# Kernel optimization log

Measured on AMD Instinct MI355X. Metric: run time of the kernel, lower is better.

Reference implementation:

```python
import jax, jax.numpy as jnp
import numpy as np

D_MODEL = 768
H = 12
D_K = D_MODEL // H
NEG = -1e9


def setup_inputs() -> dict:
    key = jax.random.key(0)
    ks = jax.random.split(key, 12)
    B, S = 1, 4096
    q = jax.random.normal(ks[0], (B, S, D_MODEL), dtype=jnp.float32)
    k = jax.random.normal(ks[1], (B, S, D_MODEL), dtype=jnp.float32)
    v = jax.random.normal(ks[2], (B, S, D_MODEL), dtype=jnp.float32)
    # causal mask, 1 = attend, 0 = masked (masked_fill on mask == 0)
    mask = jnp.tril(jnp.ones((S, S), dtype=jnp.int32))[None, None, :, :]
    scale = 1.0 / np.sqrt(D_MODEL)
    Wq = jax.random.normal(ks[3], (D_MODEL, D_MODEL), dtype=jnp.float32) * scale
    bq = jnp.zeros((D_MODEL,), dtype=jnp.float32)
    Wk = jax.random.normal(ks[4], (D_MODEL, D_MODEL), dtype=jnp.float32) * scale
    bk = jnp.zeros((D_MODEL,), dtype=jnp.float32)
    Wv = jax.random.normal(ks[5], (D_MODEL, D_MODEL), dtype=jnp.float32) * scale
    bv = jnp.zeros((D_MODEL,), dtype=jnp.float32)
    Wo = jax.random.normal(ks[6], (D_MODEL, D_MODEL), dtype=jnp.float32) * scale
    bo = jnp.zeros((D_MODEL,), dtype=jnp.float32)
    return {"q": q, "k": k, "v": v, "mask": mask,
            "Wq": Wq, "bq": bq, "Wk": Wk, "bk": bk,
            "Wv": Wv, "bv": bv, "Wo": Wo, "bo": bo}


def _split_heads(x):
    B, S, _ = x.shape
    return x.reshape(B, S, H, D_K).transpose(0, 2, 1, 3)  # [B,H,S,Dk]


def reference(q, k, v, mask, Wq, bq, Wk, bk, Wv, bv, Wo, bo):
    # Linear projections (torch Linear: x @ W.T + b; here W stored as [in,out])
    query = _split_heads(q @ Wq + bq)
    key = _split_heads(k @ Wk + bk)
    value = _split_heads(v @ Wv + bv)
    # scaled dot-product attention, full score matrix [B,H,Sq,Sk]
    scores = jnp.einsum("bhqd,bhkd->bhqk", query, key) / jnp.sqrt(
        jnp.asarray(D_K, dtype=query.dtype))
    scores = jnp.where(mask == 0, jnp.asarray(NEG, dtype=scores.dtype), scores)
    attn = jax.nn.softmax(scores, axis=-1)  # dropout p=0.0 -> identity
    x = jnp.einsum("bhqk,bhkd->bhqd", attn, value)
    B, _, S, _ = x.shape
    x = x.transpose(0, 2, 1, 3).reshape(B, S, H * D_K)
    return x @ Wo + bo
```

## Files before the change

kernel.cpp:

```cpp
#include <hip/hip_runtime.h>

typedef __bf16 bf16;
typedef __bf16 bf16x4 __attribute__((ext_vector_type(4)));
typedef __bf16 bf16x8 __attribute__((ext_vector_type(8)));
typedef float  floatx4 __attribute__((ext_vector_type(4)));

#define MFMA16(a,b,c) __builtin_amdgcn_mfma_f32_16x16x32_bf16((a),(b),(c),0,0,0)

static constexpr int S_LEN = 4096;
static constexpr int DM = 768;
static constexpr int NH = 12;
static constexpr int W_ELEMS = 768 * 768;
static constexpr int PARTS_PER_HEAD = 144;
static constexpr float CE = 0.18033688011112042f;

__device__ __forceinline__ void gld16(const bf16* g, bf16* l) {
    __builtin_amdgcn_global_load_lds(
        (const __attribute__((address_space(1))) void*)g,
        (__attribute__((address_space(3))) void*)l, 16, 0, 0);
}

__global__ __launch_bounds__(256) void prep_kernel(
    const float* __restrict__ q, const float* __restrict__ k, const float* __restrict__ v,
    const float* __restrict__ W0, const float* __restrict__ W1,
    const float* __restrict__ W2, const float* __restrict__ W3,
    bf16* Qc, bf16* Kc, bf16* Vc,
    bf16* T0, bf16* T1, bf16* T2, bf16* T3, int n)
{
    const int y = blockIdx.y;
    const int tid = threadIdx.x;
    if (y < 3) {
        const float* src = y == 0 ? q : (y == 1 ? k : v);
        bf16* dst = y == 0 ? Qc : (y == 1 ? Kc : Vc);
        int i = (blockIdx.x * 256 + tid) * 4;
        if (i < n) {
            float4 w = *(const float4*)&src[i];
            bf16x4 o; o[0] = (bf16)w.x; o[1] = (bf16)w.y; o[2] = (bf16)w.z; o[3] = (bf16)w.w;
            *(bf16x4*)&dst[i] = o;
        }
        return;
    }
    int x = blockIdx.x;
    if (x >= 576) return;
    const int mat = x / 144, t = x % 144;
    const float* W = mat == 0 ? W0 : (mat == 1 ? W1 : (mat == 2 ? W2 : W3));
    bf16* T = mat == 0 ? T0 : (mat == 1 ? T1 : (mat == 2 ? T2 : T3));
    const int k0 = (t / 12) * 64, n0 = (t % 12) * 64;
    __shared__ float Tl[64][65];
#pragma unroll
    for (int i = 0; i < 4; ++i) {
        int idx = i * 256 + tid;
        int r = idx >> 4, c4 = idx & 15;
        float4 w = *(const float4*)&W[(k0 + r) * 768 + n0 + c4 * 4];
        Tl[c4 * 4 + 0][r] = w.x; Tl[c4 * 4 + 1][r] = w.y;
        Tl[c4 * 4 + 2][r] = w.z; Tl[c4 * 4 + 3][r] = w.w;
    }
    __syncthreads();
#pragma unroll
    for (int i = 0; i < 4; ++i) {
        int idx = i * 256 + tid;
        int c = idx >> 4, r4 = idx & 15;
        bf16x4 o;
        o[0] = (bf16)Tl[c][r4 * 4 + 0]; o[1] = (bf16)Tl[c][r4 * 4 + 1];
        o[2] = (bf16)Tl[c][r4 * 4 + 2]; o[3] = (bf16)Tl[c][r4 * 4 + 3];
        *(bf16x4*)&T[(n0 + c) * 768 + k0 + r4 * 4] = o;
    }
}

template <bool OUT_F32>
__global__ __launch_bounds__(256) void gemm128_kernel(
    const bf16* __restrict__ A0, const bf16* __restrict__ A1, const bf16* __restrict__ A2,
    const bf16* __restrict__ B0, const bf16* __restrict__ B1, const bf16* __restrict__ B2,
    const float* __restrict__ c0, const float* __restrict__ c1, const float* __restrict__ c2,
    void* O0, void* O1, void* O2, int M, int N, int K, float qscale)
{
    const int z = blockIdx.z;
    const bf16* A = z == 0 ? A0 : (z == 1 ? A1 : A2);
    const bf16* B = z == 0 ? B0 : (z == 1 ? B1 : B2);
    const float* bias = z == 0 ? c0 : (z == 1 ? c1 : c2);
    void* C = z == 0 ? O0 : (z == 1 ? O1 : O2);
    const float osc = (z == 0) ? qscale : 1.0f;

    __shared__ bf16 As[2][128 * 64];
    __shared__ bf16 Bs[2][128 * 64];
    const int tid = threadIdx.x, lane = tid & 63, wave = tid >> 6;
    const int quad = lane >> 4, l16 = lane & 15, l8 = l16 & 7;
    const int rw = wave >> 1, cw = wave & 1;
    const int m0 = blockIdx.x * 128, n0 = blockIdx.y * 128;

    floatx4 acc[4][4] = {};

    auto stage = [&](int kt, int buf) {
#pragma unroll
        for (int i = 0; i < 4; ++i) {
            int ch = i * 256 + tid;
            int m = ch >> 3, kg = ch & 7;
            int kgd = kg ^ (m & 7);
            gld16(A + (size_t)(m0 + m) * K + kt * 64 + kgd * 8, &As[buf][ch * 8]);
        }
#pragma unroll
        for (int i = 0; i < 4; ++i) {
            int ch = i * 256 + tid;
            int n = ch >> 3, kg = ch & 7;
            int kgd = kg ^ (n & 7);
            gld16(B + (size_t)(n0 + n) * K + kt * 64 + kgd * 8, &Bs[buf][ch * 8]);
        }
    };

    const int NT = K >> 6;
    stage(0, 0);
    __syncthreads();

    for (int kt = 0; kt < NT; ++kt) {
        const int cur = kt & 1;
        if (kt + 1 < NT) stage(kt + 1, cur ^ 1);
#pragma unroll
        for (int ks = 0; ks < 2; ++ks) {
            bf16x8 a[4], b[4];
#pragma unroll
            for (int mt = 0; mt < 4; ++mt)
                a[mt] = *(const bf16x8*)&As[cur][(rw * 64 + mt * 16 + l16) * 64 + (((ks * 4 + quad) ^ l8) << 3)];
#pragma unroll
            for (int nt = 0; nt < 4; ++nt)
                b[nt] = *(const bf16x8*)&Bs[cur][(cw * 64 + nt * 16 + l16) * 64 + (((ks * 4 + quad) ^ l8) << 3)];
#pragma unroll
            for (int mt = 0; mt < 4; ++mt)
#pragma unroll
                for (int nt = 0; nt < 4; ++nt)
                    acc[mt][nt] = MFMA16(a[mt], b[nt], acc[mt][nt]);
        }
        __syncthreads();
    }
#pragma unroll
    for (int mt = 0; mt < 4; ++mt) {
        int row = m0 + rw * 64 + mt * 16 + quad * 4;
#pragma unroll
        for (int nt = 0; nt < 4; ++nt) {
            int col = n0 + cw * 64 + nt * 16 + l16;
            float bv = bias[col];
#pragma unroll
            for (int r = 0; r < 4; ++r) {
                float v = (acc[mt][nt][r] + bv) * osc;
                if (OUT_F32) ((float*)C)[(size_t)(row + r) * N + col] = v;
                else         ((bf16*)C)[(size_t)(row + r) * N + col] = (bf16)v;
            }
        }
    }
}

__global__ __launch_bounds__(256) void attn_kernel(
    const bf16* __restrict__ Q, const bf16* __restrict__ K,
    const bf16* __restrict__ V, float* __restrict__ Opart,
    float* __restrict__ Lpart)
{
    __shared__ bf16 Ps[128 * 64];
    __shared__ bf16 Ks[2][64 * 64];
    __shared__ bf16 Vt[64 * 64];

    const int h = blockIdx.y;
    const int idx = PARTS_PER_HEAD - 1 - (int)blockIdx.x;
    int g = 0;
    while (2 * (g + 1) * (g + 2) <= idx) ++g;
    const int rem = idx - 2 * g * (g + 1);
    const int qb = 4 * g + rem / (g + 1);
    const int c  = rem % (g + 1);
    const int ntiles = 2 * qb + 2;
    const int jstart = c * 8;
    const int jend   = (jstart + 8 < ntiles) ? jstart + 8 : ntiles;

    const int tid = threadIdx.x, lane = tid & 63, wave = tid >> 6;
    const int quad = lane >> 4, l16 = lane & 15, l8 = l16 & 7;
    const int qrow0 = qb * 128;
    const int cb = h * 64;

    auto stageK = [&](int j, int buf) {
#pragma unroll
        for (int i = 0; i < 2; ++i) {
            int ch = i * 256 + tid;
            int row = ch >> 3, kg = ch & 7;
            int kgd = kg ^ (row & 7);
            gld16(K + (size_t)(j * 64 + row) * DM + cb + kgd * 8, &Ks[buf][ch * 8]);
        }
    };
    auto loadV = [&](int j, bf16 vr[2][8]) {
#pragma unroll
        for (int i = 0; i < 2; ++i) {
            int kg = wave + i * 4;
#pragma unroll
            for (int u = 0; u < 8; ++u)
                vr[i][u] = V[(size_t)(j * 64 + kg * 8 + u) * DM + cb + lane];
        }
    };
    auto writeV = [&](bf16 vr[2][8]) {
#pragma unroll
        for (int i = 0; i < 2; ++i) {
            int kg = wave + i * 4;
            bf16x8 t;
#pragma unroll
            for (int u = 0; u < 8; ++u) t[u] = vr[i][u];
            *(bf16x8*)&Vt[lane * 64 + ((kg ^ (lane & 7)) << 3)] = t;
        }
    };

    bf16x8 qreg[2][2];
#pragma unroll
    for (int mt = 0; mt < 2; ++mt)
#pragma unroll
        for (int ks = 0; ks < 2; ++ks)
            qreg[mt][ks] = *(const bf16x8*)&Q[(size_t)(qrow0 + wave * 32 + mt * 16 + l16) * DM
                                             + cb + ks * 32 + quad * 8];

    stageK(jstart, 0);
    bf16 v0[2][8];
    loadV(jstart, v0);
    writeV(v0);
    __syncthreads();

    floatx4 o[2][4] = {};
    float lsum[2] = {0.f, 0.f};
    const int prowbase = (wave * 32 + l16) * 64;
    const int psub = (quad & 1) * 4;
    const int c16base = (quad >> 1);

    for (int j = jstart; j < jend; ++j) {
        const int cur = (j - jstart) & 1;
        bf16 vr[2][8];
        if (j + 1 < jend) {
            stageK(j + 1, cur ^ 1);
            loadV(j + 1, vr);
        }

        floatx4 st[2][4] = {};
#pragma unroll
        for (int ks = 0; ks < 2; ++ks) {
            bf16x8 kfr[4];
#pragma unroll
            for (int ct = 0; ct < 4; ++ct)
                kfr[ct] = *(const bf16x8*)&Ks[cur][(ct * 16 + l16) * 64 + (((ks * 4 + quad) ^ l8) << 3)];
#pragma unroll
            for (int mt = 0; mt < 2; ++mt)
#pragma unroll
                for (int ct = 0; ct < 4; ++ct)
                    st[mt][ct] = MFMA16(kfr[ct], qreg[mt][ks], st[mt][ct]);
        }

#pragma unroll
        for (int mt = 0; mt < 2; ++mt) {
            const int qs0 = qrow0 + wave * 32 + mt * 16;
            const int pb = prowbase + mt * 16 * 64;
            float lp = 0.f;
            if ((j * 64 + 63) <= qs0) {
#pragma unroll
                for (int ct = 0; ct < 4; ++ct) {
                    bf16x4 pk;
#pragma unroll
                    for (int r = 0; r < 4; ++r) {
                        float p = __builtin_amdgcn_exp2f(st[mt][ct][r]);
                        lp += p; pk[r] = (bf16)p;
                    }
                    *(bf16x4*)&Ps[pb + ((((ct * 2 + c16base) ^ l8) << 3) + psub)] = pk;
                }
            } else {
                const int qg = qs0 + l16;
#pragma unroll
                for (int ct = 0; ct < 4; ++ct) {
                    const int kg0 = j * 64 + ct * 16 + quad * 4;
                    bf16x4 pk;
#pragma unroll
                    for (int r = 0; r < 4; ++r) {
                        float p = (kg0 + r > qg) ? 0.f
                                  : __builtin_amdgcn_exp2f(st[mt][ct][r]);
                        lp += p; pk[r] = (bf16)p;
                    }
                    *(bf16x4*)&Ps[pb + ((((ct * 2 + c16base) ^ l8) << 3) + psub)] = pk;
                }
            }
            lsum[mt] += lp;
        }

#pragma unroll
        for (int ks = 0; ks < 2; ++ks) {
            bf16x8 bfr[4], afr[2];
#pragma unroll
            for (int ct = 0; ct < 4; ++ct)
                bfr[ct] = *(const bf16x8*)&Vt[(ct * 16 + l16) * 64 + (((ks * 4 + quad) ^ l8) << 3)];
#pragma unroll
            for (int mt = 0; mt < 2; ++mt)
                afr[mt] = *(const bf16x8*)&Ps[(wave * 32 + mt * 16 + l16) * 64 + (((ks * 4 + quad) ^ l8) << 3)];
#pragma unroll
            for (int mt = 0; mt < 2; ++mt)
#pragma unroll
                for (int ct = 0; ct < 4; ++ct)
                    o[mt][ct] = MFMA16(afr[mt], bfr[ct], o[mt][ct]);
        }

        if (j + 1 < jend) {
            __syncthreads();
            writeV(vr);
            __syncthreads();
        }
    }

    float* Op = Opart + (size_t)(h * PARTS_PER_HEAD + idx) * 128 * 64;
    float* Lp = Lpart + (size_t)(h * PARTS_PER_HEAD + idx) * 128;
#pragma unroll
    for (int mt = 0; mt < 2; ++mt) {
        float l = lsum[mt];
        l += __shfl_xor(l, 16);
        l += __shfl_xor(l, 32);
        if (lane < 16) Lp[wave * 32 + mt * 16 + l16] = l;
#pragma unroll
        for (int r = 0; r < 4; ++r) {
            const int rl = wave * 32 + mt * 16 + quad * 4 + r;
#pragma unroll
            for (int ct = 0; ct < 4; ++ct)
                Op[rl * 64 + ct * 16 + l16] = o[mt][ct][r];
        }
    }
}

__global__ __launch_bounds__(256) void attn_combine_kernel(
    const float* __restrict__ Opart, const float* __restrict__ Lpart,
    bf16* __restrict__ X)
{
    const int qb = blockIdx.x, h = blockIdx.y;
    const int g = qb >> 2;
    const int nc = g + 1;
    const int base = 2 * g * (g + 1) + (qb & 3) * (g + 1);
    const float* Op0 = Opart + (size_t)(h * PARTS_PER_HEAD + base) * 128 * 64;
    const float* Lp0 = Lpart + (size_t)(h * PARTS_PER_HEAD + base) * 128;

    for (int e = threadIdx.x * 4; e < 128 * 64; e += 1024) {
        const int row = e >> 6, col = e & 63;
        float4 acc = {0.f, 0.f, 0.f, 0.f};
        float l = 0.f;
        for (int p = 0; p < nc; ++p) {
            float4 w = *(const float4*)&Op0[p * 128 * 64 + e];
            acc.x += w.x; acc.y += w.y; acc.z += w.z; acc.w += w.w;
            l += Lp0[p * 128 + row];
        }
        const float rl = 1.0f / l;
        bf16x4 ov;
        ov[0] = (bf16)(acc.x * rl); ov[1] = (bf16)(acc.y * rl);
        ov[2] = (bf16)(acc.z * rl); ov[3] = (bf16)(acc.w * rl);
        *(bf16x4*)&X[(size_t)(qb * 128 + row) * DM + h * 64 + col] = ov;
    }
}

extern "C" void kernel_launch(void* const* d_in, const int* in_sizes, int n_in,
                              void* d_out, int out_size, void* d_ws, size_t ws_size,
                              hipStream_t stream)
{
    const float* q  = (const float*)d_in[0];
    const float* k  = (const float*)d_in[1];
    const float* v  = (const float*)d_in[2];
    const float* Wq = (const float*)d_in[4];
    const float* bq = (const float*)d_in[5];
    const float* Wk = (const float*)d_in[6];
    const float* bk = (const float*)d_in[7];
    const float* Wv = (const float*)d_in[8];
    const float* bv = (const float*)d_in[9];
    const float* Wo = (const float*)d_in[10];
    const float* bo = (const float*)d_in[11];

    const size_t NE = (size_t)S_LEN * DM;
    bf16* base = (bf16*)d_ws;
    bf16* Qp = base;
    bf16* Kp = base + NE;
    bf16* Vp = base + 2 * NE;
    bf16* Wt = base + 3 * NE;
    bf16 *Wqt = Wt, *Wkt = Wt + W_ELEMS, *Wvt = Wt + 2 * W_ELEMS, *Wot = Wt + 3 * W_ELEMS;
    bf16* scratch = Wt + 4 * W_ELEMS;
    bf16* Qc = scratch;
    bf16* Kc = scratch + NE;
    bf16* Vc = scratch + 2 * NE;
    float* Opart = (float*)scratch;
    float* Lpart = Opart + (size_t)NH * PARTS_PER_HEAD * 128 * 64;
    bf16* Xb = Qp;

    prep_kernel<<<dim3(3072, 4), 256, 0, stream>>>(
        q, k, v, Wq, Wk, Wv, Wo, Qc, Kc, Vc, Wqt, Wkt, Wvt, Wot, (int)NE);
    gemm128_kernel<false><<<dim3(32, 6, 3), 256, 0, stream>>>(
        Qc, Kc, Vc, Wqt, Wkt, Wvt, bq, bk, bv, Qp, Kp, Vp, S_LEN, DM, DM, CE);
    attn_kernel<<<dim3(PARTS_PER_HEAD, NH), 256, 0, stream>>>(Qp, Kp, Vp, Opart, Lpart);
    attn_combine_kernel<<<dim3(32, NH), 256, 0, stream>>>(Opart, Lpart, Xb);
    gemm128_kernel<true><<<dim3(32, 6, 1), 256, 0, stream>>>(
        Xb, Xb, Xb, Wot, Wot, Wot, bo, bo, bo, d_out, d_out, d_out, S_LEN, DM, DM, 1.0f);
}
```

Baseline: 276.5 us.

## Pre-transpose V globally and double-buffer V tiles via async LDS loads

Adds a separate kernel that transposes the projected V into a head-major [D, S] layout. The attention kernel can then stage V tiles with async global-to-LDS loads into a double buffer, just as it does for K. This removes the per-element scalar V loads, the register-to-LDS transpose writes and one of two barriers per iteration. Partial outputs are also stored in bf16 instead of fp32, which halves combine traffic at some precision cost, and the transpose adds an extra launch and a full pass over V.

```diff
diff --git a/kernel.cpp b/kernel.cpp
--- a/kernel.cpp
+++ b/kernel.cpp
@@ -67,6 +67,32 @@
     }
 }
 
+__global__ __launch_bounds__(256) void vtrans_kernel(
+    const bf16* __restrict__ Vp, bf16* __restrict__ VpT)
+{
+    __shared__ bf16 Tl[64][66];
+    const int tid = threadIdx.x;
+    const int r0 = blockIdx.x * 64, c0 = blockIdx.y * 64;
+#pragma unroll
+    for (int i = 0; i < 4; ++i) {
+        int idx = i * 256 + tid;
+        int r = idx >> 4, c4 = idx & 15;
+        bf16x4 w = *(const bf16x4*)&Vp[(size_t)(r0 + r) * DM + c0 + c4 * 4];
+        Tl[c4 * 4 + 0][r] = w[0]; Tl[c4 * 4 + 1][r] = w[1];
+        Tl[c4 * 4 + 2][r] = w[2]; Tl[c4 * 4 + 3][r] = w[3];
+    }
+    __syncthreads();
+#pragma unroll
+    for (int i = 0; i < 4; ++i) {
+        int idx = i * 256 + tid;
+        int c = idx >> 4, r4 = idx & 15;
+        bf16x4 o;
+        o[0] = Tl[c][r4 * 4 + 0]; o[1] = Tl[c][r4 * 4 + 1];
+        o[2] = Tl[c][r4 * 4 + 2]; o[3] = Tl[c][r4 * 4 + 3];
+        *(bf16x4*)&VpT[(size_t)(c0 + c) * S_LEN + r0 + r4 * 4] = o;
+    }
+}
+
 template <bool OUT_F32>
 __global__ __launch_bounds__(256) void gemm128_kernel(
     const bf16* __restrict__ A0, const bf16* __restrict__ A1, const bf16* __restrict__ A2,
@@ -150,12 +176,12 @@
 
 __global__ __launch_bounds__(256) void attn_kernel(
     const bf16* __restrict__ Q, const bf16* __restrict__ K,
-    const bf16* __restrict__ V, float* __restrict__ Opart,
+    const bf16* __restrict__ VpT, bf16* __restrict__ Opart,
     float* __restrict__ Lpart)
 {
     __shared__ bf16 Ps[128 * 64];
     __shared__ bf16 Ks[2][64 * 64];
-    __shared__ bf16 Vt[64 * 64];
+    __shared__ bf16 Vt[2][64 * 64];
 
     const int h = blockIdx.y;
     const int idx = PARTS_PER_HEAD - 1 - (int)blockIdx.x;
@@ -173,7 +199,7 @@
     const int qrow0 = qb * 128;
     const int cb = h * 64;
 
-    auto stageK = [&](int j, int buf) {
+    auto stageKV = [&](int j, int buf) {
 #pragma unroll
         for (int i = 0; i < 2; ++i) {
             int ch = i * 256 + tid;
@@ -181,24 +207,12 @@
             int kgd = kg ^ (row & 7);
             gld16(K + (size_t)(j * 64 + row) * DM + cb + kgd * 8, &Ks[buf][ch * 8]);
         }
-    };
-    auto loadV = [&](int j, bf16 vr[2][8]) {
 #pragma unroll
         for (int i = 0; i < 2; ++i) {
-            int kg = wave + i * 4;
-#pragma unroll
-            for (int u = 0; u < 8; ++u)
-                vr[i][u] = V[(size_t)(j * 64 + kg * 8 + u) * DM + cb + lane];
-        }
-    };
-    auto writeV = [&](bf16 vr[2][8]) {
-#pragma unroll
-        for (int i = 0; i < 2; ++i) {
-            int kg = wave + i * 4;
-            bf16x8 t;
-#pragma unroll
-            for (int u = 0; u < 8; ++u) t[u] = vr[i][u];
-            *(bf16x8*)&Vt[lane * 64 + ((kg ^ (lane & 7)) << 3)] = t;
+            int ch = i * 256 + tid;
+            int row = ch >> 3, kg = ch & 7;
+            int kgd = kg ^ (row & 7);
+            gld16(VpT + (size_t)(cb + row) * S_LEN + j * 64 + kgd * 8, &Vt[buf][ch * 8]);
         }
     };
 
@@ -210,10 +224,7 @@
             qreg[mt][ks] = *(const bf16x8*)&Q[(size_t)(qrow0 + wave * 32 + mt * 16 + l16) * DM
                                              + cb + ks * 32 + quad * 8];
 
-    stageK(jstart, 0);
-    bf16 v0[2][8];
-    loadV(jstart, v0);
-    writeV(v0);
+    stageKV(jstart, 0);
     __syncthreads();
 
     floatx4 o[2][4] = {};
@@ -224,11 +235,7 @@
 
     for (int j = jstart; j < jend; ++j) {
         const int cur = (j - jstart) & 1;
-        bf16 vr[2][8];
-        if (j + 1 < jend) {
-            stageK(j + 1, cur ^ 1);
-            loadV(j + 1, vr);
-        }
+        if (j + 1 < jend) stageKV(j + 1, cur ^ 1);
 
         floatx4 st[2][4] = {};
 #pragma unroll
@@ -283,7 +290,7 @@
             bf16x8 bfr[4], afr[2];
 #pragma unroll
             for (int ct = 0; ct < 4; ++ct)
-                bfr[ct] = *(const bf16x8*)&Vt[(ct * 16 + l16) * 64 + (((ks * 4 + quad) ^ l8) << 3)];
+                bfr[ct] = *(const bf16x8*)&Vt[cur][(ct * 16 + l16) * 64 + (((ks * 4 + quad) ^ l8) << 3)];
 #pragma unroll
             for (int mt = 0; mt < 2; ++mt)
                 afr[mt] = *(const bf16x8*)&Ps[(wave * 32 + mt * 16 + l16) * 64 + (((ks * 4 + quad) ^ l8) << 3)];
@@ -294,14 +301,10 @@
                     o[mt][ct] = MFMA16(afr[mt], bfr[ct], o[mt][ct]);
         }
 
-        if (j + 1 < jend) {
-            __syncthreads();
-            writeV(vr);
-            __syncthreads();
-        }
-    }
-
-    float* Op = Opart + (size_t)(h * PARTS_PER_HEAD + idx) * 128 * 64;
+        __syncthreads();
+    }
+
+    bf16* Op = Opart + (size_t)(h * PARTS_PER_HEAD + idx) * 128 * 64;
     float* Lp = Lpart + (size_t)(h * PARTS_PER_HEAD + idx) * 128;
 #pragma unroll
     for (int mt = 0; mt < 2; ++mt) {
@@ -314,20 +317,20 @@
             const int rl = wave * 32 + mt * 16 + quad * 4 + r;
 #pragma unroll
             for (int ct = 0; ct < 4; ++ct)
-                Op[rl * 64 + ct * 16 + l16] = o[mt][ct][r];
+                Op[rl * 64 + ct * 16 + l16] = (bf16)o[mt][ct][r];
         }
     }
 }
 
 __global__ __launch_bounds__(256) void attn_combine_kernel(
-    const float* __restrict__ Opart, const float* __restrict__ Lpart,
+    const bf16* __restrict__ Opart, const float* __restrict__ Lpart,
     bf16* __restrict__ X)
 {
     const int qb = blockIdx.x, h = blockIdx.y;
     const int g = qb >> 2;
     const int nc = g + 1;
     const int base = 2 * g * (g + 1) + (qb & 3) * (g + 1);
-    const float* Op0 = Opart + (size_t)(h * PARTS_PER_HEAD + base) * 128 * 64;
+    const bf16* Op0 = Opart + (size_t)(h * PARTS_PER_HEAD + base) * 128 * 64;
     const float* Lp0 = Lpart + (size_t)(h * PARTS_PER_HEAD + base) * 128;
 
     for (int e = threadIdx.x * 4; e < 128 * 64; e += 1024) {
@@ -335,8 +338,9 @@
         float4 acc = {0.f, 0.f, 0.f, 0.f};
         float l = 0.f;
         for (int p = 0; p < nc; ++p) {
-            float4 w = *(const float4*)&Op0[p * 128 * 64 + e];
-            acc.x += w.x; acc.y += w.y; acc.z += w.z; acc.w += w.w;
+            bf16x4 w = *(const bf16x4*)&Op0[p * 128 * 64 + e];
+            acc.x += (float)w[0]; acc.y += (float)w[1];
+            acc.z += (float)w[2]; acc.w += (float)w[3];
             l += Lp0[p * 128 + row];
         }
         const float rl = 1.0f / l;
@@ -370,19 +374,21 @@
     bf16* Vp = base + 2 * NE;
     bf16* Wt = base + 3 * NE;
     bf16 *Wqt = Wt, *Wkt = Wt + W_ELEMS, *Wvt = Wt + 2 * W_ELEMS, *Wot = Wt + 3 * W_ELEMS;
-    bf16* scratch = Wt + 4 * W_ELEMS;
+    bf16* VpT = Wt + 4 * W_ELEMS;
+    bf16* scratch = VpT + NE;
     bf16* Qc = scratch;
     bf16* Kc = scratch + NE;
     bf16* Vc = scratch + 2 * NE;
-    float* Opart = (float*)scratch;
-    float* Lpart = Opart + (size_t)NH * PARTS_PER_HEAD * 128 * 64;
+    bf16* Opart = scratch;
+    float* Lpart = (float*)(Opart + (size_t)NH * PARTS_PER_HEAD * 128 * 64);
     bf16* Xb = Qp;
 
     prep_kernel<<<dim3(3072, 4), 256, 0, stream>>>(
         q, k, v, Wq, Wk, Wv, Wo, Qc, Kc, Vc, Wqt, Wkt, Wvt, Wot, (int)NE);
     gemm128_kernel<false><<<dim3(32, 6, 3), 256, 0, stream>>>(
         Qc, Kc, Vc, Wqt, Wkt, Wvt, bq, bk, bv, Qp, Kp, Vp, S_LEN, DM, DM, CE);
-    attn_kernel<<<dim3(PARTS_PER_HEAD, NH), 256, 0, stream>>>(Qp, Kp, Vp, Opart, Lpart);
+    vtrans_kernel<<<dim3(64, 12), 256, 0, stream>>>(Vp, VpT);
+    attn_kernel<<<dim3(PARTS_PER_HEAD, NH), 256, 0, stream>>>(Qp, Kp, VpT, Opart, Lpart);
     attn_combine_kernel<<<dim3(32, NH), 256, 0, stream>>>(Opart, Lpart, Xb);
     gemm128_kernel<true><<<dim3(32, 6, 1), 256, 0, stream>>>(
         Xb, Xb, Xb, Wot, Wot, Wot, bo, bo, bo, d_out, d_out, d_out, S_LEN, DM, DM, 1.0f);
```

New measurement: 260.6 us. -5.8%, faster.
